# Kernel tuning notes

Hardware: AMD Instinct MI355X
Metric: run time of the kernel (lower is better)

## Reference

```python
import jax, jax.numpy as jnp
import numpy as np

B, C, H, W = 4, 256, 64, 64
CR = max(C // 8, 1)  # reduced channels
EPS = 1e-12  # F.normalize eps


def setup_inputs() -> dict:
    key = jax.random.key(0)
    ks = jax.random.split(key, 8)
    s = 1.0 / np.sqrt(C)
    return {
        "x": jax.random.normal(ks[0], (B, C, H, W), dtype=jnp.float32),
        "Wq": jax.random.normal(ks[1], (CR, C), dtype=jnp.float32) * s,
        "bq": jax.random.normal(ks[2], (CR,), dtype=jnp.float32) * s,
        "Wk": jax.random.normal(ks[3], (CR, C), dtype=jnp.float32) * s,
        "bk": jax.random.normal(ks[4], (CR,), dtype=jnp.float32) * s,
        "Wv": jax.random.normal(ks[5], (C, C), dtype=jnp.float32) * s,
        "bv": jax.random.normal(ks[6], (C,), dtype=jnp.float32) * s,
        "gamma": jax.random.normal(ks[7], (1,), dtype=jnp.float32),
    }


def reference(x, Wq, bq, Wk, bk, Wv, bv, gamma):
    b, c, h, w = x.shape
    xf = x.reshape(b, c, h * w)  # [B, C, N]
    # 1x1 convs are per-pixel linear maps
    q = jnp.einsum("rc,bcn->brn", Wq, xf) + bq[None, :, None]  # [B, CR, N]
    k = jnp.einsum("rc,bcn->brn", Wk, xf) + bk[None, :, None]  # [B, CR, N]
    v = jnp.einsum("dc,bcn->bdn", Wv, xf) + bv[None, :, None]  # [B, C, N]
    # attention = bmm(key^T, query): [B, N, N]
    attn = jnp.einsum("brn,brm->bnm", k, q)
    attn = jax.nn.relu(attn)
    # L1 normalize along dim=1 (rows), matching F.normalize(p=1, dim=1)
    denom = jnp.maximum(jnp.sum(jnp.abs(attn), axis=1, keepdims=True), EPS)
    attn = attn / denom
    out = jnp.einsum("bcn,bnm->bcm", v, attn).reshape(b, c, h, w)
    return gamma[0] * out + x
```

## Files before the change

kernel.cpp:

```cpp
#include <hip/hip_runtime.h>
#include <hip/hip_bf16.h>

#define NB 4
#define NC 256
#define NN 4096
#define NCR 32
#define PITCH 72

typedef __attribute__((ext_vector_type(8))) short short8_t;
typedef __attribute__((ext_vector_type(4))) float f32x4;
typedef __attribute__((ext_vector_type(2))) int int2_t;
typedef __attribute__((ext_vector_type(4))) int int4_t;
typedef __attribute__((ext_vector_type(4))) float float4_t;

static __device__ __forceinline__ unsigned short f2bf(float f) {
  unsigned u = __builtin_bit_cast(unsigned, f);
  u += 0x7FFFu + ((u >> 16) & 1u);
  return (unsigned short)(u >> 16);
}

static __device__ __forceinline__ unsigned cvt_pk(float lo, float hi) {
  unsigned r;
  asm("v_cvt_pk_bf16_f32 %0, %1, %2" : "=v"(r) : "v"(lo), "v"(hi));
  return r;
}

static __device__ __forceinline__ void lds_barrier() {
  asm volatile("s_waitcnt lgkmcnt(0)\n\ts_barrier" ::: "memory");
}

__global__ __launch_bounds__(64) void pack_w_kernel(
    const float* __restrict__ Wq, const float* __restrict__ Wk,
    const float* __restrict__ Wv, unsigned short* __restrict__ Wbf)
{
  const int row = blockIdx.x;
  const int t = threadIdx.x;
  const float* src = row < 32 ? Wq + (size_t)row * NC
                   : (row < 64 ? Wk + (size_t)(row - 32) * NC
                               : Wv + (size_t)(row - 64) * NC);
  float4_t v = *(const float4_t*)(src + t * 4);
  int2_t p;
  p[0] = cvt_pk(v[0], v[1]);
  p[1] = cvt_pk(v[2], v[3]);
  *(int2_t*)(Wbf + (size_t)row * NC + t * 4) = p;
}

__global__ __launch_bounds__(256, 2) void qkv_kernel(
    const float* __restrict__ x, const unsigned short* __restrict__ Wbf,
    const float* __restrict__ bq, const float* __restrict__ bk,
    const float* __restrict__ bv,
    unsigned short* __restrict__ Qt, unsigned short* __restrict__ Kt,
    unsigned short* __restrict__ Vt)
{
  __shared__ unsigned short xT[2][32 * 64];

  const int bid = blockIdx.x;
  const int b   = bid >> 7;
  const int m0  = (bid & 127) * 32;
  const int tid = threadIdx.x;
  const int w    = tid >> 6;
  const int lane = tid & 63;
  const int lg   = lane >> 4;
  const int lm   = lane & 15;

  const int mcol = tid & 31, kg = tid >> 5;
  const float* xld = x + (size_t)b * NC * NN + (size_t)(kg * 8) * NN + m0 + mcol;
  const int wofs = mcol * 64 + ((kg ^ (mcol & 7)) << 3);
  const unsigned short* wrow = Wbf + (size_t)(w * 80 + lm) * NC;

  const f32x4 zero4 = {0.f, 0.f, 0.f, 0.f};
  f32x4 acc[5][2];
#pragma unroll
  for (int df = 0; df < 5; df++)
#pragma unroll
    for (int mf = 0; mf < 2; mf++) acc[df][mf] = zero4;

  float xg[8], xn[8];
#pragma unroll
  for (int j = 0; j < 8; j++) xg[j] = xld[(size_t)j * NN];

#define QCHUNK(C, XC, XN, BUF) {                                              \
    if ((C) < 3) {                                                            \
      _Pragma("unroll") for (int j = 0; j < 8; j++)                           \
        XN[j] = xld[(size_t)(((C) + 1) * 64 + j) * NN];                       \
    }                                                                         \
    int4_t xwv;                                                               \
    xwv[0] = cvt_pk(XC[0], XC[1]); xwv[1] = cvt_pk(XC[2], XC[3]);             \
    xwv[2] = cvt_pk(XC[4], XC[5]); xwv[3] = cvt_pk(XC[6], XC[7]);             \
    *(int4_t*)(&xT[BUF][wofs]) = xwv;                                         \
    __syncthreads();                                                          \
    _Pragma("unroll") for (int ks = 0; ks < 2; ks++) {                        \
      short8_t xf[2];                                                         \
      _Pragma("unroll") for (int mf = 0; mf < 2; mf++) {                      \
        const int row = mf * 16 + lm;                                         \
        const int unit = (ks * 4 + lg) ^ (lm & 7);                            \
        xf[mf] = *(const short8_t*)(&xT[BUF][row * 64 + unit * 8]);           \
      }                                                                       \
      _Pragma("unroll") for (int df = 0; df < 5; df++) {                      \
        const short8_t wf = *(const short8_t*)(wrow + (size_t)df * 16 * NC +  \
                                               (C) * 64 + ks * 32 + lg * 8);  \
        _Pragma("unroll") for (int mf = 0; mf < 2; mf++)                      \
          acc[df][mf] = __builtin_amdgcn_mfma_f32_16x16x32_bf16(              \
              xf[mf], wf, acc[df][mf], 0, 0, 0);                              \
      }                                                                       \
    }                                                                         \
  }

  QCHUNK(0, xg, xn, 0)
  QCHUNK(1, xn, xg, 1)
  QCHUNK(2, xg, xn, 0)
  QCHUNK(3, xn, xg, 1)
#undef QCHUNK

#pragma unroll
  for (int df = 0; df < 5; df++) {
    const int dbase = w * 80 + df * 16;
    if (dbase < 64) {
      const bool isq = dbase < 32;
      const float bia = isq ? bq[dbase + lm] : bk[dbase - 32 + lm];
      unsigned short* dst = isq ? Qt : Kt;
      const int dcol = (isq ? dbase : dbase - 32) + lm;
#pragma unroll
      for (int mf = 0; mf < 2; mf++)
#pragma unroll
        for (int i = 0; i < 4; i++) {
          const int m = m0 + mf * 16 + lg * 4 + i;
          dst[((size_t)b * NN + m) * NCR + dcol] = f2bf(acc[df][mf][i] + bia);
        }
    } else {
      const int c = dbase - 64 + lm;
      const float bia = bv[c];
#pragma unroll
      for (int mf = 0; mf < 2; mf++) {
        int2_t p;
        p[0] = cvt_pk(acc[df][mf][0] + bia, acc[df][mf][1] + bia);
        p[1] = cvt_pk(acc[df][mf][2] + bia, acc[df][mf][3] + bia);
        *(int2_t*)(Vt + ((size_t)b * NC + c) * NN + m0 + mf * 16 + lg * 4) = p;
      }
    }
  }
}

__global__ __launch_bounds__(256, 2) void attn_kernel(
    const unsigned short* __restrict__ Qt, const unsigned short* __restrict__ Kt,
    const unsigned short* __restrict__ Vt, const float* __restrict__ x,
    const float* __restrict__ gamma, float* __restrict__ out)
{
  __shared__ unsigned short Slds[2][64 * PITCH];
  __shared__ float dlds[4][64];

  const int bid = blockIdx.x;
  const int xcd = bid & 7;
  const int b   = xcd >> 1;
  const int ch  = xcd & 1;
  const int m0  = (bid >> 3) * 64;
  const int tid = threadIdx.x;
  const int w    = tid >> 6;
  const int lane = tid & 63;
  const int lg   = lane >> 4;
  const int lm   = lane & 15;

  const unsigned short* Qb = Qt + (size_t)b * NN * NCR;
  const unsigned short* Kp = Kt + (size_t)b * NN * NCR +
                             (size_t)(w * 16 + lm) * NCR + lg * 8;
  const unsigned short* pV[2];
#pragma unroll
  for (int cf = 0; cf < 2; cf++)
    pV[cf] = Vt + ((size_t)b * NC + ch * 128 + w * 32 + cf * 16 + lm) * NN + lg * 8;

  short8_t qf[4];
#pragma unroll
  for (int mf = 0; mf < 4; mf++)
    qf[mf] = *(const short8_t*)(Qb + (size_t)(m0 + mf * 16 + lm) * NCR + lg * 8);

  const f32x4 zero4 = {0.f, 0.f, 0.f, 0.f};
  f32x4 acc[2][4];
#pragma unroll
  for (int cf = 0; cf < 2; cf++)
#pragma unroll
    for (int mf = 0; mf < 4; mf++) acc[cf][mf] = zero4;
  float dsum[4] = {0.f, 0.f, 0.f, 0.f};

  const int swofs = w * 16 + lg * 4;

#define SCOMP(KREG, WB) {                                                     \
    _Pragma("unroll") for (int mf = 0; mf < 4; mf++) {                        \
      f32x4 s = __builtin_amdgcn_mfma_f32_16x16x32_bf16(KREG, qf[mf], zero4, 0, 0, 0); \
      float s0 = fmaxf(s[0], 0.f), s1 = fmaxf(s[1], 0.f);                     \
      float s2 = fmaxf(s[2], 0.f), s3 = fmaxf(s[3], 0.f);                     \
      dsum[mf] += (s0 + s1) + (s2 + s3);                                      \
      int2_t p; p[0] = cvt_pk(s0, s1); p[1] = cvt_pk(s2, s3);                 \
      *(int2_t*)(&Slds[WB][(mf * 16 + lm) * PITCH + swofs]) = p;              \
    }                                                                         \
  }

  short8_t kA, kB, vA[2][2], vB[2][2];
  {
    const short8_t k0 = *(const short8_t*)(Kp);
    SCOMP(k0, 0)
  }
  kA = *(const short8_t*)(Kp + (size_t)64 * NCR);
#pragma unroll
  for (int cf = 0; cf < 2; cf++) {
    vA[cf][0] = *(const short8_t*)(pV[cf]);
    vA[cf][1] = *(const short8_t*)(pV[cf] + 32);
  }
  lds_barrier();

#define ITER(T, KU, KF, VU, VF, WB, RB, DOS) {                                \
    const int nk = (((T) + 2) & 63) * 64;                                     \
    KF = *(const short8_t*)(Kp + (size_t)nk * NCR);                           \
    const int nv = (((T) + 1) & 63) * 64;                                     \
    _Pragma("unroll") for (int cf = 0; cf < 2; cf++) {                        \
      VF[cf][0] = *(const short8_t*)(pV[cf] + nv);                            \
      VF[cf][1] = *(const short8_t*)(pV[cf] + nv + 32);                       \
    }                                                                         \
    if (DOS) { SCOMP(KU, WB) }                                                \
    __builtin_amdgcn_s_setprio(1);                                            \
    _Pragma("unroll") for (int nch = 0; nch < 2; nch++) {                     \
      short8_t sf[4];                                                         \
      _Pragma("unroll") for (int mf = 0; mf < 4; mf++)                        \
        sf[mf] = *(const short8_t*)(&Slds[RB][(mf * 16 + lm) * PITCH +        \
                                             nch * 32 + lg * 8]);             \
      _Pragma("unroll") for (int cf = 0; cf < 2; cf++)                        \
        _Pragma("unroll") for (int mf = 0; mf < 4; mf++)                      \
          acc[cf][mf] = __builtin_amdgcn_mfma_f32_16x16x32_bf16(              \
              VU[cf][nch], sf[mf], acc[cf][mf], 0, 0, 0);                     \
    }                                                                         \
    __builtin_amdgcn_s_setprio(0);                                            \
    lds_barrier();                                                            \
  }

#pragma unroll 1
  for (int t = 0; t < 62; t += 2) {
    ITER(t, kA, kB, vA, vB, 1, 0, true)
    ITER(t + 1, kB, kA, vB, vA, 0, 1, true)
  }
  ITER(62, kA, kB, vA, vB, 1, 0, true)
  ITER(63, kB, kA, vB, vA, 0, 1, false)
#undef ITER
#undef SCOMP

#pragma unroll
  for (int mf = 0; mf < 4; mf++) {
    float v = dsum[mf];
    v += __shfl_xor(v, 16);
    v += __shfl_xor(v, 32);
    if (lane < 16) dlds[w][mf * 16 + lane] = v;
  }
  __syncthreads();

  const float g0 = gamma[0];
  float rden[4];
#pragma unroll
  for (int mf = 0; mf < 4; mf++) {
    const int mloc = mf * 16 + lm;
    float den = dlds[0][mloc] + dlds[1][mloc] + dlds[2][mloc] + dlds[3][mloc];
    den = den > 1e-12f ? den : 1e-12f;
    rden[mf] = 1.0f / den;
  }

  const float* xb = x + (size_t)b * NC * NN;
  float* ob = out + (size_t)b * NC * NN;
#pragma unroll
  for (int cf = 0; cf < 2; cf++) {
#pragma unroll
    for (int i = 0; i < 4; i++) {
      const int c = ch * 128 + w * 32 + cf * 16 + lg * 4 + i;
#pragma unroll
      for (int mf = 0; mf < 4; mf++) {
        const int m = m0 + mf * 16 + lm;
        ob[(size_t)c * NN + m] = g0 * acc[cf][mf][i] * rden[mf] + xb[(size_t)c * NN + m];
      }
    }
  }
}

extern "C" void kernel_launch(void* const* d_in, const int* in_sizes, int n_in,
                              void* d_out, int out_size, void* d_ws, size_t ws_size,
                              hipStream_t stream) {
  const float* x     = (const float*)d_in[0];
  const float* Wq    = (const float*)d_in[1];
  const float* bq    = (const float*)d_in[2];
  const float* Wk    = (const float*)d_in[3];
  const float* bk    = (const float*)d_in[4];
  const float* Wv    = (const float*)d_in[5];
  const float* bv    = (const float*)d_in[6];
  const float* gamma = (const float*)d_in[7];
  float* out = (float*)d_out;

  unsigned short* Wbf = (unsigned short*)d_ws;
  unsigned short* Qt  = Wbf + (size_t)320 * NC;
  unsigned short* Kt  = Qt + (size_t)NB * NN * NCR;
  unsigned short* Vt  = Kt + (size_t)NB * NN * NCR;

  hipLaunchKernelGGL(pack_w_kernel, dim3(320), dim3(64), 0, stream,
                     Wq, Wk, Wv, Wbf);
  hipLaunchKernelGGL(qkv_kernel, dim3(512), dim3(256), 0, stream,
                     x, Wbf, bq, bk, bv, Qt, Kt, Vt);
  hipLaunchKernelGGL(attn_kernel, dim3(512), dim3(256), 0, stream,
                     Qt, Kt, Vt, x, gamma, out);
}
```

Baseline: 94.54 us.

## Double attention tile width to 128 keys per iteration and drop V prefetch

```diff
diff --git a/kernel.cpp b/kernel.cpp
--- a/kernel.cpp
+++ b/kernel.cpp
@@ -5,7 +5,7 @@
 #define NC 256
 #define NN 4096
 #define NCR 32
-#define PITCH 72
+#define PITCH2 136
 
 typedef __attribute__((ext_vector_type(8))) short short8_t;
 typedef __attribute__((ext_vector_type(4))) float f32x4;
@@ -146,7 +146,7 @@
     const unsigned short* __restrict__ Vt, const float* __restrict__ x,
     const float* __restrict__ gamma, float* __restrict__ out)
 {
-  __shared__ unsigned short Slds[2][64 * PITCH];
+  __shared__ unsigned short Slds[2][64 * PITCH2];
   __shared__ float dlds[4][64];
 
   const int bid = blockIdx.x;
@@ -181,63 +181,58 @@
     for (int mf = 0; mf < 4; mf++) acc[cf][mf] = zero4;
   float dsum[4] = {0.f, 0.f, 0.f, 0.f};
 
-  const int swofs = w * 16 + lg * 4;
-
-#define SCOMP(KREG, WB) {                                                     \
+#define SCOMP(KREG, WB, NSOFF) {                                              \
     _Pragma("unroll") for (int mf = 0; mf < 4; mf++) {                        \
       f32x4 s = __builtin_amdgcn_mfma_f32_16x16x32_bf16(KREG, qf[mf], zero4, 0, 0, 0); \
       float s0 = fmaxf(s[0], 0.f), s1 = fmaxf(s[1], 0.f);                     \
       float s2 = fmaxf(s[2], 0.f), s3 = fmaxf(s[3], 0.f);                     \
       dsum[mf] += (s0 + s1) + (s2 + s3);                                      \
       int2_t p; p[0] = cvt_pk(s0, s1); p[1] = cvt_pk(s2, s3);                 \
-      *(int2_t*)(&Slds[WB][(mf * 16 + lm) * PITCH + swofs]) = p;              \
-    }                                                                         \
-  }
-
-  short8_t kA, kB, vA[2][2], vB[2][2];
+      *(int2_t*)(&Slds[WB][(mf * 16 + lm) * PITCH2 + (NSOFF) + w * 16 + lg * 4]) = p; \
+    }                                                                         \
+  }
+
+  short8_t kA0, kA1, kB0, kB1;
   {
-    const short8_t k0 = *(const short8_t*)(Kp);
-    SCOMP(k0, 0)
-  }
-  kA = *(const short8_t*)(Kp + (size_t)64 * NCR);
-#pragma unroll
-  for (int cf = 0; cf < 2; cf++) {
-    vA[cf][0] = *(const short8_t*)(pV[cf]);
-    vA[cf][1] = *(const short8_t*)(pV[cf] + 32);
-  }
+    const short8_t k00 = *(const short8_t*)(Kp);
+    const short8_t k01 = *(const short8_t*)(Kp + (size_t)64 * NCR);
+    SCOMP(k00, 0, 0)
+    SCOMP(k01, 0, 64)
+  }
+  kA0 = *(const short8_t*)(Kp + (size_t)128 * NCR);
+  kA1 = *(const short8_t*)(Kp + (size_t)192 * NCR);
   lds_barrier();
 
-#define ITER(T, KU, KF, VU, VF, WB, RB, DOS) {                                \
-    const int nk = (((T) + 2) & 63) * 64;                                     \
-    KF = *(const short8_t*)(Kp + (size_t)nk * NCR);                           \
-    const int nv = (((T) + 1) & 63) * 64;                                     \
-    _Pragma("unroll") for (int cf = 0; cf < 2; cf++) {                        \
-      VF[cf][0] = *(const short8_t*)(pV[cf] + nv);                            \
-      VF[cf][1] = *(const short8_t*)(pV[cf] + nv + 32);                       \
-    }                                                                         \
-    if (DOS) { SCOMP(KU, WB) }                                                \
-    __builtin_amdgcn_s_setprio(1);                                            \
-    _Pragma("unroll") for (int nch = 0; nch < 2; nch++) {                     \
+#define ITER(T, KC0, KC1, KN0, KN1, WB, RB, DOS) {                            \
+    const int nv = (T) * 128;                                                 \
+    short8_t vc[2][4];                                                        \
+    _Pragma("unroll") for (int cf = 0; cf < 2; cf++)                          \
+      _Pragma("unroll") for (int nch = 0; nch < 4; nch++)                     \
+        vc[cf][nch] = *(const short8_t*)(pV[cf] + nv + nch * 32);             \
+    const int nk = (((T) + 2) & 31) * 128;                                    \
+    KN0 = *(const short8_t*)(Kp + (size_t)nk * NCR);                          \
+    KN1 = *(const short8_t*)(Kp + (size_t)(nk + 64) * NCR);                   \
+    if (DOS) { SCOMP(KC0, WB, 0) SCOMP(KC1, WB, 64) }                         \
+    _Pragma("unroll") for (int nch = 0; nch < 4; nch++) {                     \
       short8_t sf[4];                                                         \
       _Pragma("unroll") for (int mf = 0; mf < 4; mf++)                        \
-        sf[mf] = *(const short8_t*)(&Slds[RB][(mf * 16 + lm) * PITCH +        \
+        sf[mf] = *(const short8_t*)(&Slds[RB][(mf * 16 + lm) * PITCH2 +       \
                                              nch * 32 + lg * 8]);             \
       _Pragma("unroll") for (int cf = 0; cf < 2; cf++)                        \
         _Pragma("unroll") for (int mf = 0; mf < 4; mf++)                      \
           acc[cf][mf] = __builtin_amdgcn_mfma_f32_16x16x32_bf16(              \
-              VU[cf][nch], sf[mf], acc[cf][mf], 0, 0, 0);                     \
-    }                                                                         \
-    __builtin_amdgcn_s_setprio(0);                                            \
+              vc[cf][nch], sf[mf], acc[cf][mf], 0, 0, 0);                     \
+    }                                                                         \
     lds_barrier();                                                            \
   }
 
 #pragma unroll 1
-  for (int t = 0; t < 62; t += 2) {
-    ITER(t, kA, kB, vA, vB, 1, 0, true)
-    ITER(t + 1, kB, kA, vB, vA, 0, 1, true)
-  }
-  ITER(62, kA, kB, vA, vB, 1, 0, true)
-  ITER(63, kB, kA, vB, vA, 0, 1, false)
+  for (int t = 0; t < 30; t += 2) {
+    ITER(t, kA0, kA1, kB0, kB1, 1, 0, true)
+    ITER(t + 1, kB0, kB1, kA0, kA1, 0, 1, true)
+  }
+  ITER(30, kA0, kA1, kB0, kB1, 1, 0, true)
+  ITER(31, kB0, kB1, kA0, kA1, 0, 1, false)
 #undef ITER
 #undef SCOMP
 
```

Measured after the change: 97.22 us. +2.8%, slower.

## Retile attention kernel to 128-pixel query tiles with 64-channel quarters and padded V

Applied to the files above, without the earlier changes.

```diff
diff --git a/kernel.cpp b/kernel.cpp
--- a/kernel.cpp
+++ b/kernel.cpp
@@ -6,6 +6,7 @@
 #define NN 4096
 #define NCR 32
 #define PITCH 72
+#define VP (NN + 32)
 
 typedef __attribute__((ext_vector_type(8))) short short8_t;
 typedef __attribute__((ext_vector_type(4))) float f32x4;
@@ -135,7 +136,7 @@
         int2_t p;
         p[0] = cvt_pk(acc[df][mf][0] + bia, acc[df][mf][1] + bia);
         p[1] = cvt_pk(acc[df][mf][2] + bia, acc[df][mf][3] + bia);
-        *(int2_t*)(Vt + ((size_t)b * NC + c) * NN + m0 + mf * 16 + lg * 4) = p;
+        *(int2_t*)(Vt + (size_t)(b * NC + c) * VP + m0 + mf * 16 + lg * 4) = p;
       }
     }
   }
@@ -146,14 +147,17 @@
     const unsigned short* __restrict__ Vt, const float* __restrict__ x,
     const float* __restrict__ gamma, float* __restrict__ out)
 {
-  __shared__ unsigned short Slds[2][64 * PITCH];
-  __shared__ float dlds[4][64];
+  __shared__ unsigned short Slds[2][128 * PITCH];
+  __shared__ float dlds[4][128];
 
   const int bid = blockIdx.x;
   const int xcd = bid & 7;
+  const int idx = bid >> 3;
   const int b   = xcd >> 1;
-  const int ch  = xcd & 1;
-  const int m0  = (bid >> 3) * 64;
+  const int cq  = (xcd & 1) * 2 + (idx & 1);
+  const int mt  = idx >> 1;
+  const int m0  = mt * 128;
+  const int cbase = cq * 64;
   const int tid = threadIdx.x;
   const int w    = tid >> 6;
   const int lane = tid & 63;
@@ -163,28 +167,23 @@
   const unsigned short* Qb = Qt + (size_t)b * NN * NCR;
   const unsigned short* Kp = Kt + (size_t)b * NN * NCR +
                              (size_t)(w * 16 + lm) * NCR + lg * 8;
-  const unsigned short* pV[2];
-#pragma unroll
-  for (int cf = 0; cf < 2; cf++)
-    pV[cf] = Vt + ((size_t)b * NC + ch * 128 + w * 32 + cf * 16 + lm) * NN + lg * 8;
-
-  short8_t qf[4];
-#pragma unroll
-  for (int mf = 0; mf < 4; mf++)
+  const unsigned short* pV = Vt + (size_t)(b * NC + cbase + w * 16 + lm) * VP + lg * 8;
+
+  short8_t qf[8];
+#pragma unroll
+  for (int mf = 0; mf < 8; mf++)
     qf[mf] = *(const short8_t*)(Qb + (size_t)(m0 + mf * 16 + lm) * NCR + lg * 8);
 
   const f32x4 zero4 = {0.f, 0.f, 0.f, 0.f};
-  f32x4 acc[2][4];
-#pragma unroll
-  for (int cf = 0; cf < 2; cf++)
-#pragma unroll
-    for (int mf = 0; mf < 4; mf++) acc[cf][mf] = zero4;
-  float dsum[4] = {0.f, 0.f, 0.f, 0.f};
+  f32x4 acc[8];
+#pragma unroll
+  for (int mf = 0; mf < 8; mf++) acc[mf] = zero4;
+  float dsum[8] = {0.f, 0.f, 0.f, 0.f, 0.f, 0.f, 0.f, 0.f};
 
   const int swofs = w * 16 + lg * 4;
 
 #define SCOMP(KREG, WB) {                                                     \
-    _Pragma("unroll") for (int mf = 0; mf < 4; mf++) {                        \
+    _Pragma("unroll") for (int mf = 0; mf < 8; mf++) {                        \
       f32x4 s = __builtin_amdgcn_mfma_f32_16x16x32_bf16(KREG, qf[mf], zero4, 0, 0, 0); \
       float s0 = fmaxf(s[0], 0.f), s1 = fmaxf(s[1], 0.f);                     \
       float s2 = fmaxf(s[2], 0.f), s3 = fmaxf(s[3], 0.f);                     \
@@ -194,40 +193,32 @@
     }                                                                         \
   }
 
-  short8_t kA, kB, vA[2][2], vB[2][2];
+  short8_t kA, kB, vA[2], vB[2];
   {
     const short8_t k0 = *(const short8_t*)(Kp);
     SCOMP(k0, 0)
   }
   kA = *(const short8_t*)(Kp + (size_t)64 * NCR);
-#pragma unroll
-  for (int cf = 0; cf < 2; cf++) {
-    vA[cf][0] = *(const short8_t*)(pV[cf]);
-    vA[cf][1] = *(const short8_t*)(pV[cf] + 32);
-  }
+  vA[0] = *(const short8_t*)(pV);
+  vA[1] = *(const short8_t*)(pV + 32);
   lds_barrier();
 
 #define ITER(T, KU, KF, VU, VF, WB, RB, DOS) {                                \
     const int nk = (((T) + 2) & 63) * 64;                                     \
     KF = *(const short8_t*)(Kp + (size_t)nk * NCR);                           \
     const int nv = (((T) + 1) & 63) * 64;                                     \
-    _Pragma("unroll") for (int cf = 0; cf < 2; cf++) {                        \
-      VF[cf][0] = *(const short8_t*)(pV[cf] + nv);                            \
-      VF[cf][1] = *(const short8_t*)(pV[cf] + nv + 32);                       \
-    }                                                                         \
+    VF[0] = *(const short8_t*)(pV + nv);                                      \
+    VF[1] = *(const short8_t*)(pV + nv + 32);                                 \
     if (DOS) { SCOMP(KU, WB) }                                                \
-    __builtin_amdgcn_s_setprio(1);                                            \
     _Pragma("unroll") for (int nch = 0; nch < 2; nch++) {                     \
-      short8_t sf[4];                                                         \
-      _Pragma("unroll") for (int mf = 0; mf < 4; mf++)                        \
+      short8_t sf[8];                                                         \
+      _Pragma("unroll") for (int mf = 0; mf < 8; mf++)                        \
         sf[mf] = *(const short8_t*)(&Slds[RB][(mf * 16 + lm) * PITCH +        \
                                              nch * 32 + lg * 8]);             \
-      _Pragma("unroll") for (int cf = 0; cf < 2; cf++)                        \
-        _Pragma("unroll") for (int mf = 0; mf < 4; mf++)                      \
-          acc[cf][mf] = __builtin_amdgcn_mfma_f32_16x16x32_bf16(              \
-              VU[cf][nch], sf[mf], acc[cf][mf], 0, 0, 0);                     \
-    }                                                                         \
-    __builtin_amdgcn_s_setprio(0);                                            \
+      _Pragma("unroll") for (int mf = 0; mf < 8; mf++)                        \
+        acc[mf] = __builtin_amdgcn_mfma_f32_16x16x32_bf16(                    \
+            VU[nch], sf[mf], acc[mf], 0, 0, 0);                               \
+    }                                                                         \
     lds_barrier();                                                            \
   }
 
@@ -242,7 +233,7 @@
 #undef SCOMP
 
 #pragma unroll
-  for (int mf = 0; mf < 4; mf++) {
+  for (int mf = 0; mf < 8; mf++) {
     float v = dsum[mf];
     v += __shfl_xor(v, 16);
     v += __shfl_xor(v, 32);
@@ -251,9 +242,9 @@
   __syncthreads();
 
   const float g0 = gamma[0];
-  float rden[4];
-#pragma unroll
-  for (int mf = 0; mf < 4; mf++) {
+  float rden[8];
+#pragma unroll
+  for (int mf = 0; mf < 8; mf++) {
     const int mloc = mf * 16 + lm;
     float den = dlds[0][mloc] + dlds[1][mloc] + dlds[2][mloc] + dlds[3][mloc];
     den = den > 1e-12f ? den : 1e-12f;
@@ -263,15 +254,12 @@
   const float* xb = x + (size_t)b * NC * NN;
   float* ob = out + (size_t)b * NC * NN;
 #pragma unroll
-  for (int cf = 0; cf < 2; cf++) {
-#pragma unroll
-    for (int i = 0; i < 4; i++) {
-      const int c = ch * 128 + w * 32 + cf * 16 + lg * 4 + i;
-#pragma unroll
-      for (int mf = 0; mf < 4; mf++) {
-        const int m = m0 + mf * 16 + lm;
-        ob[(size_t)c * NN + m] = g0 * acc[cf][mf][i] * rden[mf] + xb[(size_t)c * NN + m];
-      }
+  for (int i = 0; i < 4; i++) {
+    const int c = cbase + w * 16 + lg * 4 + i;
+#pragma unroll
+    for (int mf = 0; mf < 8; mf++) {
+      const int m = m0 + mf * 16 + lm;
+      ob[(size_t)c * NN + m] = g0 * acc[mf][i] * rden[mf] + xb[(size_t)c * NN + m];
     }
   }
 }
```

After: 92.83 us. Within noise of the previous version (-1.8%).
